# Optimization experiments

Measured on AMD Instinct MI355X. Metric: run time of the kernel, lower is better.

## Reference

```python
import jax, jax.numpy as jnp
import numpy as np

B, N, M, DIM = 64, 512, 512, 64
GAMMA = 1.0
BANDWIDTH = 0.0  # 0 => Sakoe-Chiba pruning disabled (bandwidth=None in torch module)
BIG = 1e10       # finite stand-in for +inf boundary; exp(-BIG/gamma) underflows to 0


def setup_inputs() -> dict:
    key = jax.random.key(0)
    kx, ky, kl = jax.random.split(key, 3)
    X = jax.random.normal(kx, (B, N, DIM), dtype=jnp.float32)
    Y = jax.random.normal(ky, (B, M, DIM), dtype=jnp.float32)
    # valid lengths in [N//2, N]
    lengths_x = jax.random.randint(kl, (B,), N // 2, N + 1, dtype=jnp.int32)
    return {"X": X, "Y": Y, "lengths_x": lengths_x}


def _pairwise_sq_dist(x, y):
    # D[b,i,j] = sum_d (x[b,i,d] - y[b,j,d])^2, via the gemm expansion to
    # avoid materializing a [B,N,M,D] tensor.
    x2 = jnp.sum(x * x, axis=-1)[:, :, None]            # [B,N,1]
    y2 = jnp.sum(y * y, axis=-1)[:, None, :]            # [B,1,M]
    xy = jnp.einsum("bnd,bmd->bnm", x, y)               # [B,N,M]
    return x2 + y2 - 2.0 * xy


def _softdtw(D, lengths):
    # Anti-diagonal wavefront DP. Diagonal k holds R[i, k-i] (1-based DP grid,
    # R[0,0]=0, all other boundary cells = BIG (stand-in for +inf)).
    Bb, Nn, Mm = D.shape
    ivec = jnp.arange(Nn + 1)                            # storage index i = 0..N
    rows = jnp.clip(ivec - 1, 0, Nn - 1)                 # D row index (static)
    len_mask = ivec[None, :] <= lengths[:, None]         # rows i>L stay at inf

    d_km2 = jnp.full((Bb, Nn + 1), BIG, D.dtype).at[:, 0].set(0.0)  # diag k=0
    d_km1 = jnp.full((Bb, Nn + 1), BIG, D.dtype)                     # diag k=1

    def step(carry, k):
        d2, d1 = carry
        j = k - ivec                                     # (N+1,)
        cols = jnp.clip(j - 1, 0, Mm - 1)
        Dk = D[:, rows, cols]                            # D[b, i-1, j-1] -> (B, N+1)
        # neighbors: d2[i-1]=R[i-1,j-1], d1[i-1]=R[i-1,j], d1[i]=R[i,j-1]
        r0 = -jnp.roll(d2, 1, axis=1) / GAMMA
        r1 = -jnp.roll(d1, 1, axis=1) / GAMMA
        r2 = -d1 / GAMMA
        softmin = -GAMMA * jax.nn.logsumexp(jnp.stack([r0, r1, r2]), axis=0)
        valid = (ivec >= 1) & (j >= 1) & (j <= Mm)
        if BANDWIDTH > 0:
            valid = valid & (jnp.abs(ivec - j) <= BANDWIDTH)
        valid = valid[None, :] & len_mask
        new = jnp.where(valid, Dk + softmin, BIG)
        return (d1, new), new

    ks = jnp.arange(2, Nn + Mm + 1)
    _, diags = jax.lax.scan(step, (d_km2, d_km1), ks)    # (N+M-1, B, N+1)
    # R[b, L_b, M] lives on diagonal k = L_b + M (scan index k-2) at position i=L_b
    return diags[lengths + Mm - 2, jnp.arange(Bb), lengths]


def reference(X, Y, lengths_x):
    D = _pairwise_sq_dist(X, Y)
    return _softdtw(D, lengths_x)
```

## Files before the change

### kernel.cpp

```cpp
#include <hip/hip_runtime.h>

constexpr int Bc   = 64;
constexpr int Nc   = 512;
constexpr int Mc   = 512;
constexpr int DIMc = 64;
constexpr float BIGc = 1e10f;
constexpr int CELLS = Nc * Mc;
constexpr float LOG2E = 1.442695041f;
constexpr float LN2   = 0.6931471806f;

struct TrueC  { static constexpr bool value = true;  };
struct FalseC { static constexpr bool value = false; };

typedef __attribute__((ext_vector_type(8))) short short8v;
typedef __attribute__((ext_vector_type(4))) float f32x4;

__device__ __forceinline__ int diag_off(int g) {
    if (g < Mc) return g * (g + 1) / 2;
    int e = g - Mc;
    return Mc * (Mc + 1) / 2 + e * (Nc - 1) - e * (e - 1) / 2;
}
__device__ __forceinline__ int diag_nmin(int g) {
    return (g > Mc - 1) ? (g - (Mc - 1)) : 0;
}
__device__ __forceinline__ int dOffm(int g) {
    if (g < 512) return g * (g + 1) / 2;
    int e = g - 512;
    return 131328 + e * 511 - e * (e - 1) / 2 - (g - 511);
}

__device__ __forceinline__ unsigned short f2bf_rne(float f) {
    unsigned u = __builtin_bit_cast(unsigned, f);
    u += 0x7FFFu + ((u >> 16) & 1u);
    return (unsigned short)(u >> 16);
}
__device__ __forceinline__ float bf2f(unsigned short h) {
    return __builtin_bit_cast(float, (unsigned)h << 16);
}

__device__ __forceinline__ float dpp_shr1_f(float v, float old) {
    return __builtin_bit_cast(float, __builtin_amdgcn_update_dpp(
        __builtin_bit_cast(int, old), __builtin_bit_cast(int, v), 0x138, 0xF, 0xF, false));
}
__device__ __forceinline__ float f4c(const float4 v, int c) {
    switch (c & 3) { case 0: return v.x; case 1: return v.y;
                     case 2: return v.z; default: return v.w; }
}
__device__ __forceinline__ void f4set(float4& d, int c, float v) {
    switch (c & 3) { case 0: d.x = v; break; case 1: d.y = v; break;
                     case 2: d.z = v; break; default: d.w = v; }
}

__global__ __launch_bounds__(256)
void compute_D_mfma(const float* __restrict__ X, const float* __restrict__ Y,
                    unsigned short* __restrict__ Dc)
{
    __shared__ unsigned short Xs[128 * 72];
    __shared__ unsigned short Ys[128 * 72];
    __shared__ unsigned short Ct[128 * 132];
    __shared__ float xn2[128], ym2[128];

    const int b   = blockIdx.x;
    const int nt  = blockIdx.y >> 2;
    const int mt_ = blockIdx.y & 3;
    const int n0  = nt * 128, m0 = mt_ * 128;
    const int tid = threadIdx.x;

    const float* Xb = X + ((size_t)b * Nc + n0) * DIMc;
    const float* Yb = Y + ((size_t)b * Mc + m0) * DIMc;
    unsigned short* Db = Dc + (size_t)b * CELLS;

    {
        const float4* Xb4 = reinterpret_cast<const float4*>(Xb);
        const float4* Yb4 = reinterpret_cast<const float4*>(Yb);
        #pragma unroll
        for (int it = 0; it < 8; ++it) {
            const int c4 = tid + it * 256;
            const int row = c4 >> 4, k4 = (c4 & 15) * 4;
            float4 xv = Xb4[c4];
            float4 yv = Yb4[c4];
            ushort4 xs = make_ushort4(f2bf_rne(xv.x), f2bf_rne(xv.y),
                                      f2bf_rne(xv.z), f2bf_rne(xv.w));
            ushort4 ys = make_ushort4(f2bf_rne(yv.x), f2bf_rne(yv.y),
                                      f2bf_rne(yv.z), f2bf_rne(yv.w));
            *reinterpret_cast<ushort4*>(&Xs[row * 72 + k4]) = xs;
            *reinterpret_cast<ushort4*>(&Ys[row * 72 + k4]) = ys;
        }
    }
    __syncthreads();

    {
        const int rr = tid & 127;
        const unsigned short* src = (tid < 128) ? Xs : Ys;
        float s = 0.f;
        #pragma unroll
        for (int kk = 0; kk < 64; ++kk) {
            float v = bf2f(src[rr * 72 + kk]);
            s = fmaf(v, v, s);
        }
        if (tid < 128) xn2[rr] = s; else ym2[rr] = s;
    }
    __syncthreads();

    const int w    = __builtin_amdgcn_readfirstlane(tid >> 6);
    const int lane = tid & 63;
    const int wr = w >> 1, wc = w & 1;
    const int lo = lane & 15, hi = lane >> 4;

    f32x4 acc[4][4];
    #pragma unroll
    for (int ri = 0; ri < 4; ++ri)
        #pragma unroll
        for (int ci = 0; ci < 4; ++ci) acc[ri][ci] = f32x4{0.f, 0.f, 0.f, 0.f};

    #pragma unroll
    for (int ks = 0; ks < 2; ++ks) {
        short8v a[4], bf[4];
        const int kb = ks * 32 + hi * 8;
        #pragma unroll
        for (int ri = 0; ri < 4; ++ri)
            a[ri] = *reinterpret_cast<const short8v*>(
                        &Xs[(wr * 64 + ri * 16 + lo) * 72 + kb]);
        #pragma unroll
        for (int ci = 0; ci < 4; ++ci)
            bf[ci] = *reinterpret_cast<const short8v*>(
                        &Ys[(wc * 64 + ci * 16 + lo) * 72 + kb]);
        #pragma unroll
        for (int ri = 0; ri < 4; ++ri)
            #pragma unroll
            for (int ci = 0; ci < 4; ++ci)
                acc[ri][ci] = __builtin_amdgcn_mfma_f32_16x16x32_bf16(
                                  a[ri], bf[ci], acc[ri][ci], 0, 0, 0);
    }

    #pragma unroll
    for (int ri = 0; ri < 4; ++ri)
        #pragma unroll
        for (int ci = 0; ci < 4; ++ci)
            #pragma unroll
            for (int rg = 0; rg < 4; ++rg) {
                const int row = wr * 64 + ri * 16 + hi * 4 + rg;
                const int col = wc * 64 + ci * 16 + lo;
                float val = fmaf(-2.f, acc[ri][ci][rg], xn2[row] + ym2[col]) * LOG2E;
                Ct[row * 132 + col] = f2bf_rne(val);
            }
    __syncthreads();

    const int grp = tid >> 6;
    const int g00 = n0 + m0;
    for (int d = grp; d < 255; d += 4) {
        const int tn_lo = max(0, d - 127);
        const int tn_hi = min(127, d);
        const int dg    = g00 + d;
        const int base  = dOffm(dg) + n0;
        for (int o = lane; o <= tn_hi - tn_lo; o += 64) {
            const int tn = tn_lo + o;
            Db[base + tn] = Ct[tn * 132 + (d - tn)];
        }
    }
}

__global__ __launch_bounds__(512)
void softdtw_sys16(const unsigned short* __restrict__ Dch,
                   const int* __restrict__ lengths, float* __restrict__ out)
{
    __shared__ float ring[8][64];
    const int b    = blockIdx.x;
    const int t    = threadIdx.x;
    const int lane = t & 63;
    const int W    = __builtin_amdgcn_readfirstlane(t >> 6);
    const int L    = lengths[b];
    const int r    = (W << 6) + lane;
    const unsigned short* Dbat = Dch + (size_t)b * CELLS;

    if (t < 64) ring[0][t] = BIGc;
    __syncthreads();

    const bool l0   = (lane == 0);
    const bool iok  = (r <= L - 1);
    const int  gcap = (r == L - 1) ? (L + 510) : -1;
    const int  qlL  = (L + 510) >> 4;
    const bool rowsOK = ((W << 6) + 64) <= L;
    const int  q0 = 4 * W;
    const int  ql = min(4 * W + 35, qlL);
    const int  cmax = qlL + 8;

    float own = BIGc, nb1 = BIGc, nb2 = BIGc, res = 0.f;
    if (W == 0 && l0) nb2 = 0.f;

    unsigned Dwin[16];
    {
        int sb = dOffm(q0 * 16);
        int gg = q0 * 16;
        #pragma unroll
        for (int s = 0; s < 16; ++s) {
            Dwin[s] = Dbat[sb + r];
            int d1 = (gg < 512) ? (gg + 1) : (1023 - gg);
            sb += d1 - ((gg >= 511) ? 1 : 0);
            ++gg;
        }
    }

    for (int c = 0; c < cmax; ++c) {
        const int q = c - W;
        if (q >= q0 && q <= ql) {
            const int g0 = q * 16;
            const int rbase = g0 & 63;

            float Df[16];
            #pragma unroll
            for (int s = 0; s < 16; ++s)
                Df[s] = __builtin_bit_cast(float, Dwin[s] << 16);

            float4 rv[4];
            {
                const float4* rp = reinterpret_cast<const float4*>(&ring[W][rbase]);
                #pragma unroll
                for (int u = 0; u < 4; ++u) rv[u] = rp[u];
            }

            const bool doNext = (q + 1 <= ql);
            int gN  = doNext ? (g0 + 16) : 0;
            int sbN = dOffm(gN);

            float4 expv[4];
            const bool fastC = rowsOK && q >= q0 + 4 && q <= q0 + 31 && q != qlL;

            auto body = [&](auto FASTC) {
                constexpr bool FAST = decltype(FASTC)::value;
                #pragma unroll
                for (int s = 0; s < 16; ++s) {
                    const int g = g0 + s;
                    const float mn = fminf(nb2, fminf(nb1, own));
                    const float e  = __builtin_amdgcn_exp2f(mn - nb2)
                                   + __builtin_amdgcn_exp2f(mn - nb1)
                                   + __builtin_amdgcn_exp2f(mn - own);
                    const float sm = mn - __builtin_amdgcn_logf(e);
                    float v = Df[s] + sm;
                    if (!FAST) {
                        const bool jok = (unsigned)(g - r) < (unsigned)Mc;
                        v = (jok && iok) ? v : BIGc;
                        res = (g == gcap) ? v : res;
                    }
                    Dwin[s] = Dbat[sbN + r];
                    {
                        int d1 = (gN < 512) ? (gN + 1) : (1023 - gN);
                        sbN += d1 - ((gN >= 511) ? 1 : 0);
                        ++gN;
                    }
                    f4set(expv[s >> 2], s, v);
                    const float sh = dpp_shr1_f(v, BIGc);
                    nb2 = nb1;
                    nb1 = l0 ? f4c(rv[s >> 2], s) : sh;
                    own = v;
                }
            };
            if (fastC) body(TrueC{}); else body(FalseC{});

            if (W < 7 && lane == 63) {
                float* re = &ring[W + 1][rbase];
                #pragma unroll
                for (int u = 0; u < 4; ++u)
                    reinterpret_cast<float4*>(re)[u] = expv[u];
            }
        } else if (W > 0 && q == q0 - 1) {
            nb1 = l0 ? ring[W][63] : nb1;
            nb2 = l0 ? ring[W][62] : nb2;
        }
        asm volatile("s_waitcnt lgkmcnt(0)" ::: "memory");
        __builtin_amdgcn_s_barrier();
        asm volatile("" ::: "memory");
    }

    if (r == L - 1) out[b] = res * LN2;
}

__global__ __launch_bounds__(512)
void softdtw_fused(const float* __restrict__ X, const float* __restrict__ Y,
                   const int* __restrict__ lengths, float* __restrict__ out)
{
    const int b = blockIdx.x;
    const int t = threadIdx.x;
    const int i = t + 1;
    const int L = lengths[b];

    __shared__ float diag[3][Nc + 1];
    for (int c = t; c <= Nc; c += 512) {
        diag[0][c] = (c == 0) ? 0.f : BIGc;
        diag[1][c] = BIGc;
    }
    float xr[DIMc];
    const float* Xrow = X + ((size_t)b * Nc + t) * DIMc;
    #pragma unroll
    for (int d = 0; d < DIMc; d += 4) {
        float4 v = *reinterpret_cast<const float4*>(Xrow + d);
        xr[d] = v.x; xr[d+1] = v.y; xr[d+2] = v.z; xr[d+3] = v.w;
    }
    const float* Yb = Y + (size_t)b * Mc * DIMc;
    __syncthreads();

    float result = BIGc;
    int cur = 2, p1 = 1, p2 = 0;
    for (int k = 2; k <= Nc + Mc; ++k) {
        const int j = k - i;
        const bool valid = (j >= 1) && (j <= Mc) && (i <= L);
        float Dval = 0.f;
        if (valid) {
            const float* Yrow = Yb + (size_t)(j - 1) * DIMc;
            float s = 0.f;
            #pragma unroll
            for (int d = 0; d < DIMc; d += 4) {
                float4 v = *reinterpret_cast<const float4*>(Yrow + d);
                float d0 = xr[d] - v.x, d1 = xr[d+1] - v.y;
                float d2 = xr[d+2] - v.z, d3 = xr[d+3] - v.w;
                s = fmaf(d0,d0,s); s = fmaf(d1,d1,s); s = fmaf(d2,d2,s); s = fmaf(d3,d3,s);
            }
            Dval = s;
        }
        const float a2 = diag[p2][i-1], a1 = diag[p1][i-1], a0 = diag[p1][i];
        const float mn = fminf(a2, fminf(a1, a0));
        const float sm = mn - __logf(__expf(mn-a2) + __expf(mn-a1) + __expf(mn-a0));
        const float val = valid ? (Dval + sm) : BIGc;
        diag[cur][i] = val;
        if (t == 0) diag[cur][0] = BIGc;
        if (k == L + Mc && i == L) result = val;
        __syncthreads();
        const int tmp = p2; p2 = p1; p1 = cur; cur = tmp;
    }
    if (i == L) out[b] = result;
}

extern "C" void kernel_launch(void* const* d_in, const int* in_sizes, int n_in,
                              void* d_out, int out_size, void* d_ws, size_t ws_size,
                              hipStream_t stream) {
    const float* X = (const float*)d_in[0];
    const float* Y = (const float*)d_in[1];
    const int* lengths = (const int*)d_in[2];
    float* out = (float*)d_out;

    const size_t need = (size_t)Bc * CELLS * sizeof(unsigned short);
    if (ws_size >= need) {
        unsigned short* Dc = (unsigned short*)d_ws;
        compute_D_mfma<<<dim3(Bc, 16), 256, 0, stream>>>(X, Y, Dc);
        softdtw_sys16<<<Bc, 512, 0, stream>>>(Dc, lengths, out);
    } else {
        softdtw_fused<<<Bc, 512, 0, stream>>>(X, Y, lengths, out);
    }
}
```

Before: 183.6 us.

## Represent soft-DTW DP cells as scaled-exponent pairs to drop per-cell log

Each DP cell is now stored as a mantissa factor F plus an integer exponent A, meaning the value is exp2(-(A - log2 F)), instead of a plain log-domain float. Soft-min then becomes an integer min, three exponent-field adds and a multiply by exp2(rint(D)-D). That replaces three exp2 calls and a log per cell with one exp2 and some integer ops, with renormalisation every four steps. The cost is twice the LDS ring traffic, an extra DPP shift for the integer part, and more registers. Clamping exponent shifts at -96 and renormalising only periodically may lose accuracy relative to the log-sum-exp form.

```diff
diff --git a/kernel.cpp b/kernel.cpp
--- a/kernel.cpp
+++ b/kernel.cpp
@@ -8,6 +8,7 @@
 constexpr int CELLS = Nc * Mc;
 constexpr float LOG2E = 1.442695041f;
 constexpr float LN2   = 0.6931471806f;
+constexpr int ALARGE = 1 << 26;
 
 struct TrueC  { static constexpr bool value = true;  };
 struct FalseC { static constexpr bool value = false; };
@@ -15,14 +16,6 @@
 typedef __attribute__((ext_vector_type(8))) short short8v;
 typedef __attribute__((ext_vector_type(4))) float f32x4;
 
-__device__ __forceinline__ int diag_off(int g) {
-    if (g < Mc) return g * (g + 1) / 2;
-    int e = g - Mc;
-    return Mc * (Mc + 1) / 2 + e * (Nc - 1) - e * (e - 1) / 2;
-}
-__device__ __forceinline__ int diag_nmin(int g) {
-    return (g > Mc - 1) ? (g - (Mc - 1)) : 0;
-}
 __device__ __forceinline__ int dOffm(int g) {
     if (g < 512) return g * (g + 1) / 2;
     int e = g - 512;
@@ -42,6 +35,9 @@
     return __builtin_bit_cast(float, __builtin_amdgcn_update_dpp(
         __builtin_bit_cast(int, old), __builtin_bit_cast(int, v), 0x138, 0xF, 0xF, false));
 }
+__device__ __forceinline__ int dpp_shr1_i(int v, int old) {
+    return __builtin_amdgcn_update_dpp(old, v, 0x138, 0xF, 0xF, false);
+}
 __device__ __forceinline__ float f4c(const float4 v, int c) {
     switch (c & 3) { case 0: return v.x; case 1: return v.y;
                      case 2: return v.z; default: return v.w; }
@@ -49,6 +45,17 @@
 __device__ __forceinline__ void f4set(float4& d, int c, float v) {
     switch (c & 3) { case 0: d.x = v; break; case 1: d.y = v; break;
                      case 2: d.z = v; break; default: d.w = v; }
+}
+__device__ __forceinline__ int i4c(const int4 v, int c) {
+    switch (c & 3) { case 0: return v.x; case 1: return v.y;
+                     case 2: return v.z; default: return v.w; }
+}
+__device__ __forceinline__ void i4set(int4& d, int c, int v) {
+    switch (c & 3) { case 0: d.x = v; break; case 1: d.y = v; break;
+                     case 2: d.z = v; break; default: d.w = v; }
+}
+__device__ __forceinline__ float expadd(float F, int s) {
+    return __builtin_bit_cast(float, __builtin_bit_cast(int, F) + (s << 23));
 }
 
 __global__ __launch_bounds__(256)
@@ -161,10 +168,11 @@
 }
 
 __global__ __launch_bounds__(512)
-void softdtw_sys16(const unsigned short* __restrict__ Dch,
+void softdtw_exp16(const unsigned short* __restrict__ Dch,
                    const int* __restrict__ lengths, float* __restrict__ out)
 {
-    __shared__ float ring[8][64];
+    __shared__ float ringF[8][64];
+    __shared__ int   ringA[8][64];
     const int b    = blockIdx.x;
     const int t    = threadIdx.x;
     const int lane = t & 63;
@@ -173,7 +181,7 @@
     const int r    = (W << 6) + lane;
     const unsigned short* Dbat = Dch + (size_t)b * CELLS;
 
-    if (t < 64) ring[0][t] = BIGc;
+    if (t < 64) { ringF[0][t] = 1.0f; ringA[0][t] = ALARGE; }
     __syncthreads();
 
     const bool l0   = (lane == 0);
@@ -185,8 +193,10 @@
     const int  ql = min(4 * W + 35, qlL);
     const int  cmax = qlL + 8;
 
-    float own = BIGc, nb1 = BIGc, nb2 = BIGc, res = 0.f;
-    if (W == 0 && l0) nb2 = 0.f;
+    float Fo = 1.0f, Fn1 = 1.0f, Fn2 = 1.0f;
+    int   Ao = ALARGE, An1 = ALARGE, An2 = ALARGE;
+    if (W == 0 && l0) { Fn2 = 1.0f; An2 = 0; }
+    float resF = 1.0f; int resA = 0;
 
     unsigned Dwin[16];
     {
@@ -207,23 +217,19 @@
             const int g0 = q * 16;
             const int rbase = g0 & 63;
 
-            float Df[16];
-            #pragma unroll
-            for (int s = 0; s < 16; ++s)
-                Df[s] = __builtin_bit_cast(float, Dwin[s] << 16);
-
-            float4 rv[4];
+            float4 rvF[4]; int4 rvA[4];
             {
-                const float4* rp = reinterpret_cast<const float4*>(&ring[W][rbase]);
+                const float4* rpF = reinterpret_cast<const float4*>(&ringF[W][rbase]);
+                const int4*   rpA = reinterpret_cast<const int4*>(&ringA[W][rbase]);
                 #pragma unroll
-                for (int u = 0; u < 4; ++u) rv[u] = rp[u];
+                for (int u = 0; u < 4; ++u) { rvF[u] = rpF[u]; rvA[u] = rpA[u]; }
             }
 
             const bool doNext = (q + 1 <= ql);
             int gN  = doNext ? (g0 + 16) : 0;
             int sbN = dOffm(gN);
 
-            float4 expv[4];
+            float4 expvF[4]; int4 expvA[4];
             const bool fastC = rowsOK && q >= q0 + 4 && q <= q0 + 31 && q != qlL;
 
             auto body = [&](auto FASTC) {
@@ -231,16 +237,31 @@
                 #pragma unroll
                 for (int s = 0; s < 16; ++s) {
                     const int g = g0 + s;
-                    const float mn = fminf(nb2, fminf(nb1, own));
-                    const float e  = __builtin_amdgcn_exp2f(mn - nb2)
-                                   + __builtin_amdgcn_exp2f(mn - nb1)
-                                   + __builtin_amdgcn_exp2f(mn - own);
-                    const float sm = mn - __builtin_amdgcn_logf(e);
-                    float v = Df[s] + sm;
+                    const float Df  = bf2f((unsigned short)Dwin[s]);
+                    const float rdf = rintf(Df);
+                    const int   rdi = (int)rdf;
+                    const float w   = __builtin_amdgcn_exp2f(rdf - Df);
+                    const int Ar = min(Ao, min(An1, An2));
+                    const int s0 = max(Ar - Ao,  -96);
+                    const int s1 = max(Ar - An1, -96);
+                    const int s2 = max(Ar - An2, -96);
+                    float F0 = expadd(Fo,  s0);
+                    float F1 = expadd(Fn1, s1);
+                    float F2 = expadd(Fn2, s2);
+                    float Fn = w * ((F0 + F1) + F2);
+                    int   An = Ar + rdi;
                     if (!FAST) {
                         const bool jok = (unsigned)(g - r) < (unsigned)Mc;
-                        v = (jok && iok) ? v : BIGc;
-                        res = (g == gcap) ? v : res;
+                        const bool valid = jok && iok;
+                        Fn = valid ? Fn : 1.0f;
+                        An = valid ? An : ALARGE;
+                        if (g == gcap) { resF = Fn; resA = An; }
+                    }
+                    if ((s & 3) == 3) {
+                        int e = ((__builtin_bit_cast(int, Fn) >> 23) & 0xFF) - 127;
+                        Fn = __builtin_bit_cast(float,
+                                 __builtin_bit_cast(int, Fn) - (e << 23));
+                        An += e;
                     }
                     Dwin[s] = Dbat[sbN + r];
                     {
@@ -248,31 +269,40 @@
                         sbN += d1 - ((gN >= 511) ? 1 : 0);
                         ++gN;
                     }
-                    f4set(expv[s >> 2], s, v);
-                    const float sh = dpp_shr1_f(v, BIGc);
-                    nb2 = nb1;
-                    nb1 = l0 ? f4c(rv[s >> 2], s) : sh;
-                    own = v;
+                    f4set(expvF[s >> 2], s, Fn);
+                    i4set(expvA[s >> 2], s, An);
+                    const float shF = dpp_shr1_f(Fn, 1.0f);
+                    const int   shA = dpp_shr1_i(An, ALARGE);
+                    Fn2 = Fn1; An2 = An1;
+                    Fn1 = l0 ? f4c(rvF[s >> 2], s) : shF;
+                    An1 = l0 ? i4c(rvA[s >> 2], s) : shA;
+                    Fo = Fn; Ao = An;
                 }
             };
             if (fastC) body(TrueC{}); else body(FalseC{});
 
             if (W < 7 && lane == 63) {
-                float* re = &ring[W + 1][rbase];
+                float* reF = &ringF[W + 1][rbase];
+                int*   reA = &ringA[W + 1][rbase];
                 #pragma unroll
-                for (int u = 0; u < 4; ++u)
-                    reinterpret_cast<float4*>(re)[u] = expv[u];
+                for (int u = 0; u < 4; ++u) {
+                    reinterpret_cast<float4*>(reF)[u] = expvF[u];
+                    reinterpret_cast<int4*>(reA)[u]   = expvA[u];
+                }
             }
         } else if (W > 0 && q == q0 - 1) {
-            nb1 = l0 ? ring[W][63] : nb1;
-            nb2 = l0 ? ring[W][62] : nb2;
+            if (l0) {
+                Fn1 = ringF[W][63]; An1 = ringA[W][63];
+                Fn2 = ringF[W][62]; An2 = ringA[W][62];
+            }
         }
         asm volatile("s_waitcnt lgkmcnt(0)" ::: "memory");
         __builtin_amdgcn_s_barrier();
         asm volatile("" ::: "memory");
     }
 
-    if (r == L - 1) out[b] = res * LN2;
+    if (r == L - 1)
+        out[b] = ((float)resA - __builtin_amdgcn_logf(resF)) * LN2;
 }
 
 __global__ __launch_bounds__(512)
@@ -342,7 +372,7 @@
     if (ws_size >= need) {
         unsigned short* Dc = (unsigned short*)d_ws;
         compute_D_mfma<<<dim3(Bc, 16), 256, 0, stream>>>(X, Y, Dc);
-        softdtw_sys16<<<Bc, 512, 0, stream>>>(Dc, lengths, out);
+        softdtw_exp16<<<Bc, 512, 0, stream>>>(Dc, lengths, out);
     } else {
         softdtw_fused<<<Bc, 512, 0, stream>>>(X, Y, lengths, out);
     }
```

New measurement: 188.0 us. 2.4% more time.
